# Kernel optimization log

Measured on AMD Instinct MI355X. Metric: run time of the kernel, lower is better.

Reference implementation:

```python
import jax, jax.numpy as jnp
import numpy as np
from jax import lax

ITERATIONS = 10
B, I, D, J, E = 512, 7, 512, 64, 128


def setup_inputs() -> dict:
    key = jax.random.key(0)
    k1, k2, k3 = jax.random.split(key, 3)
    f_bid = jax.random.normal(k1, (B, I, D), dtype=jnp.float32)
    p_bi = jax.random.uniform(k2, (B, I), dtype=jnp.float32)
    weights = jax.random.normal(k3, (I, D, J, E), dtype=jnp.float32)
    return {"f_bid": f_bid, "p_bi": p_bi, "weights": weights}


def reference(f_bid, p_bi, weights):
    # Precompute the per-capsule vote tensor once: [B, I, J, E]
    f_W_bije = jnp.einsum('bid,idje->bije', f_bid, weights)
    b = f_bid.shape[0]
    j, e = weights.shape[2], weights.shape[3]
    c0 = jnp.ones((b, j, e), dtype=f_bid.dtype)

    def body(c_bj, _):
        # routing logits over output capsules j, softmax over j (dim=-1 of 'bij')
        r_bij = jax.nn.softmax(jnp.einsum('bije,bje->bij', f_W_bije, c_bj), axis=-1)
        c_next = jnp.einsum('bi,bij,bije->bje', p_bi, r_bij, f_W_bije)
        return c_next, r_bij

    c_bj, r_stack = lax.scan(body, c0, None, length=ITERATIONS)
    return c_bj, r_stack[-1]
```

## Files before the change

kernel.cpp:

```cpp
#include <hip/hip_runtime.h>
#include <hip/hip_bf16.h>

#define B_SZ 512
#define I_SZ 7
#define D_SZ 512
#define J_SZ 64
#define E_SZ 128
#define N_SZ 8192
#define ITERS 10

typedef __attribute__((ext_vector_type(8))) short bf16x8;
typedef __attribute__((ext_vector_type(4))) float f32x4;

#if defined(__has_builtin)
#if __has_builtin(__builtin_amdgcn_cvt_pk_bf16_f32)
#define HAVE_CVT_PK_BF16 1
#endif
#endif

__device__ inline void split2(float x0, float x1, unsigned& hp, unsigned& lp) {
#ifdef HAVE_CVT_PK_BF16
    auto h = __builtin_amdgcn_cvt_pk_bf16_f32(x0, x1);
    hp = __builtin_bit_cast(unsigned, h);
    union { unsigned u; float f; } b0, b1;
    b0.u = hp << 16;
    b1.u = hp & 0xFFFF0000u;
    auto l = __builtin_amdgcn_cvt_pk_bf16_f32(x0 - b0.f, x1 - b1.f);
    lp = __builtin_bit_cast(unsigned, l);
#else
    union { float f; unsigned u; } u0, u1;
    u0.f = x0; u1.f = x1;
    unsigned r0 = u0.u + 0x7FFF + ((u0.u >> 16) & 1);
    unsigned r1 = u1.u + 0x7FFF + ((u1.u >> 16) & 1);
    hp = __builtin_amdgcn_perm(r1, r0, 0x07060302);
    union { unsigned u; float f; } h0, h1;
    h0.u = r0 & 0xFFFF0000u;
    h1.u = r1 & 0xFFFF0000u;
    union { float f; unsigned u; } s0, s1;
    s0.f = x0 - h0.f; s1.f = x1 - h1.f;
    unsigned q0 = s0.u + 0x7FFF + ((s0.u >> 16) & 1);
    unsigned q1 = s1.u + 0x7FFF + ((s1.u >> 16) & 1);
    lp = __builtin_amdgcn_perm(q1, q0, 0x07060302);
#endif
}

__global__ __launch_bounds__(256, 2) void vote_gemm_mfma(
    const float* __restrict__ f,
    const float* __restrict__ W,
    float* __restrict__ fW)
{
    const int i  = blockIdx.z;
    const int m0 = blockIdx.y * 128;
    const int n0 = blockIdx.x * 128;
    const int th = threadIdx.x;
    const int lane = th & 63;
    const int wave = th >> 6;
    const int wr   = wave >> 1;
    const int wc   = wave & 1;
    const int quad = lane >> 4;
    const int lm   = lane & 15;

    __shared__ short Ah_s[2][128 * 32];
    __shared__ short Al_s[2][128 * 32];
    __shared__ short Bh_s[2][128 * 32];
    __shared__ short Bl_s[2][128 * 32];

    const int sm = th >> 1;
    const int kh = th & 1;
    const int swz = (sm >> 1) & 3;
    const int wo0 = sm * 32 + (((kh << 1) | 0) ^ swz) * 8;
    const int wo1 = sm * 32 + (((kh << 1) | 1) ^ swz) * 8;

    const float* aPtr = f + (size_t)(m0 + sm) * (I_SZ * D_SZ) + (size_t)i * D_SZ + kh * 16;
    const float* bPtr = W + (size_t)i * D_SZ * N_SZ + (size_t)(kh * 16) * N_SZ + n0 + sm;

    const int fpos8 = (quad ^ ((lm >> 1) & 3)) * 8;

    f32x4 acc[4][4];
#pragma unroll
    for (int a = 0; a < 4; ++a)
#pragma unroll
        for (int c = 0; c < 4; ++c)
            acc[a][c] = (f32x4){0.f, 0.f, 0.f, 0.f};

    float av[16], bv[16];
    auto stage_load = [&](int kt) {
        const float* pa = aPtr + kt * 32;
        float4 t0 = *(const float4*)(pa);
        float4 t1 = *(const float4*)(pa + 4);
        float4 t2 = *(const float4*)(pa + 8);
        float4 t3 = *(const float4*)(pa + 12);
        av[0]=t0.x;  av[1]=t0.y;  av[2]=t0.z;  av[3]=t0.w;
        av[4]=t1.x;  av[5]=t1.y;  av[6]=t1.z;  av[7]=t1.w;
        av[8]=t2.x;  av[9]=t2.y;  av[10]=t2.z; av[11]=t2.w;
        av[12]=t3.x; av[13]=t3.y; av[14]=t3.z; av[15]=t3.w;
        const float* pb = bPtr + (size_t)kt * 32 * N_SZ;
#pragma unroll
        for (int r = 0; r < 16; ++r) bv[r] = pb[(size_t)r * N_SZ];
    };
    auto stage_write = [&](int slot) {
        short* qAh = &Ah_s[slot][0]; short* qAl = &Al_s[slot][0];
        short* qBh = &Bh_s[slot][0]; short* qBl = &Bl_s[slot][0];
        uint4 h, l;
        split2(av[0],  av[1],  h.x, l.x); split2(av[2],  av[3],  h.y, l.y);
        split2(av[4],  av[5],  h.z, l.z); split2(av[6],  av[7],  h.w, l.w);
        *(uint4*)&qAh[wo0] = h; *(uint4*)&qAl[wo0] = l;
        split2(av[8],  av[9],  h.x, l.x); split2(av[10], av[11], h.y, l.y);
        split2(av[12], av[13], h.z, l.z); split2(av[14], av[15], h.w, l.w);
        *(uint4*)&qAh[wo1] = h; *(uint4*)&qAl[wo1] = l;
        split2(bv[0],  bv[1],  h.x, l.x); split2(bv[2],  bv[3],  h.y, l.y);
        split2(bv[4],  bv[5],  h.z, l.z); split2(bv[6],  bv[7],  h.w, l.w);
        *(uint4*)&qBh[wo0] = h; *(uint4*)&qBl[wo0] = l;
        split2(bv[8],  bv[9],  h.x, l.x); split2(bv[10], bv[11], h.y, l.y);
        split2(bv[12], bv[13], h.z, l.z); split2(bv[14], bv[15], h.w, l.w);
        *(uint4*)&qBh[wo1] = h; *(uint4*)&qBl[wo1] = l;
    };

    stage_load(0);
    stage_write(0);
    __syncthreads();

    for (int t = 0; t < 16; ++t) {
        const int s = t & 1;
        const short* pAh = &Ah_s[s][0]; const short* pAl = &Al_s[s][0];
        const short* pBh = &Bh_s[s][0]; const short* pBl = &Bl_s[s][0];

        if (t < 15) stage_load(t + 1);
        __builtin_amdgcn_sched_barrier(0);

        bf16x8 Bf_h[4], Bf_l[4];
#pragma unroll
        for (int ns = 0; ns < 4; ++ns) {
            const int o = (wc * 64 + ns * 16 + lm) * 32 + fpos8;
            Bf_h[ns] = *(const bf16x8*)&pBh[o];
            Bf_l[ns] = *(const bf16x8*)&pBl[o];
        }
#pragma unroll
        for (int ms = 0; ms < 3; ++ms) {
            const int o = (wr * 64 + ms * 16 + lm) * 32 + fpos8;
            const bf16x8 Af_h = *(const bf16x8*)&pAh[o];
            const bf16x8 Af_l = *(const bf16x8*)&pAl[o];
            __builtin_amdgcn_s_setprio(1);
#pragma unroll
            for (int ns = 0; ns < 4; ++ns) {
                acc[ms][ns] = __builtin_amdgcn_mfma_f32_16x16x32_bf16(Af_h, Bf_h[ns], acc[ms][ns], 0, 0, 0);
                acc[ms][ns] = __builtin_amdgcn_mfma_f32_16x16x32_bf16(Af_h, Bf_l[ns], acc[ms][ns], 0, 0, 0);
                acc[ms][ns] = __builtin_amdgcn_mfma_f32_16x16x32_bf16(Af_l, Bf_h[ns], acc[ms][ns], 0, 0, 0);
            }
            __builtin_amdgcn_s_setprio(0);
        }
        __builtin_amdgcn_sched_barrier(0);

        if (t < 15) stage_write(s ^ 1);
        __builtin_amdgcn_sched_barrier(0);

        {
            const int o = (wr * 64 + 3 * 16 + lm) * 32 + fpos8;
            const bf16x8 Af_h = *(const bf16x8*)&pAh[o];
            const bf16x8 Af_l = *(const bf16x8*)&pAl[o];
            __builtin_amdgcn_s_setprio(1);
#pragma unroll
            for (int ns = 0; ns < 4; ++ns) {
                acc[3][ns] = __builtin_amdgcn_mfma_f32_16x16x32_bf16(Af_h, Bf_h[ns], acc[3][ns], 0, 0, 0);
                acc[3][ns] = __builtin_amdgcn_mfma_f32_16x16x32_bf16(Af_h, Bf_l[ns], acc[3][ns], 0, 0, 0);
                acc[3][ns] = __builtin_amdgcn_mfma_f32_16x16x32_bf16(Af_l, Bf_h[ns], acc[3][ns], 0, 0, 0);
            }
            __builtin_amdgcn_s_setprio(0);
        }
        __builtin_amdgcn_sched_barrier(0);

        __syncthreads();
    }

#pragma unroll
    for (int ms = 0; ms < 4; ++ms) {
        const int rowb = m0 + wr * 64 + ms * 16 + quad * 4;
#pragma unroll
        for (int ns = 0; ns < 4; ++ns) {
            const int col = n0 + wc * 64 + ns * 16 + lm;
#pragma unroll
            for (int r = 0; r < 4; ++r)
                fW[((size_t)(rowb + r) * I_SZ + i) * N_SZ + col] = acc[ms][ns][r];
        }
    }
}

__global__ __launch_bounds__(1024) void routing_kernel(
    const float* __restrict__ fW,
    const float* __restrict__ p,
    float* __restrict__ c_out,
    float* __restrict__ r_out)
{
    const int b   = blockIdx.x;
    const int tid = threadIdx.x;
    const int j   = tid >> 4;
    const int sub = tid & 15;

    __shared__ float G_sh[64][49];
    __shared__ float s_sh[64][9];
    __shared__ float w_sh[2][64][9];
    __shared__ float p_sh[8];

    if (tid < I_SZ) p_sh[tid] = p[(size_t)b * I_SZ + tid];

    float4 fw[I_SZ][2];
    const float* base = fW + (size_t)b * I_SZ * N_SZ + j * E_SZ + sub * 8;
#pragma unroll
    for (int i = 0; i < I_SZ; ++i) {
        fw[i][0] = *(const float4*)(base + (size_t)i * N_SZ);
        fw[i][1] = *(const float4*)(base + (size_t)i * N_SZ + 4);
    }

#pragma unroll
    for (int i = 0; i < I_SZ; ++i) {
        float s = fw[i][0].x + fw[i][0].y + fw[i][0].z + fw[i][0].w
                + fw[i][1].x + fw[i][1].y + fw[i][1].z + fw[i][1].w;
        s += __shfl_xor(s, 1); s += __shfl_xor(s, 2);
        s += __shfl_xor(s, 4); s += __shfl_xor(s, 8);
        if (sub == 0) s_sh[j][i] = s;
#pragma unroll
        for (int i2 = i; i2 < I_SZ; ++i2) {
            float g = fw[i][0].x * fw[i2][0].x + fw[i][0].y * fw[i2][0].y
                    + fw[i][0].z * fw[i2][0].z + fw[i][0].w * fw[i2][0].w
                    + fw[i][1].x * fw[i2][1].x + fw[i][1].y * fw[i2][1].y
                    + fw[i][1].z * fw[i2][1].z + fw[i][1].w * fw[i2][1].w;
            g += __shfl_xor(g, 1); g += __shfl_xor(g, 2);
            g += __shfl_xor(g, 4); g += __shfl_xor(g, 8);
            if (sub == 0) { G_sh[j][i * 7 + i2] = g; G_sh[j][i2 * 7 + i] = g; }
        }
    }
    __syncthreads();

    for (int t = 0; t < ITERS; ++t) {
        if (tid < I_SZ * 64) {
            const int ii = tid >> 6;
            const int jj = tid & 63;
            float l;
            if (t == 0) {
                l = s_sh[jj][ii];
            } else {
                const int rb = t & 1;
                l = 0.f;
#pragma unroll
                for (int i2 = 0; i2 < I_SZ; ++i2)
                    l = fmaf(w_sh[rb][jj][i2], G_sh[jj][ii * 7 + i2], l);
            }
            float mx = l;
#pragma unroll
            for (int off = 32; off > 0; off >>= 1)
                mx = fmaxf(mx, __shfl_xor(mx, off));
            float ex = __expf(l - mx);
            float sm = ex;
#pragma unroll
            for (int off = 32; off > 0; off >>= 1)
                sm += __shfl_xor(sm, off);
            float r = ex / sm;
            if (t == ITERS - 1)
                r_out[(size_t)b * (I_SZ * J_SZ) + ii * 64 + jj] = r;
            w_sh[(t + 1) & 1][jj][ii] = p_sh[ii] * r;
        }
        __syncthreads();
    }

    float4 a0 = make_float4(0.f, 0.f, 0.f, 0.f);
    float4 a1 = make_float4(0.f, 0.f, 0.f, 0.f);
#pragma unroll
    for (int i = 0; i < I_SZ; ++i) {
        float wv = w_sh[ITERS & 1][j][i];
        a0.x = fmaf(wv, fw[i][0].x, a0.x); a0.y = fmaf(wv, fw[i][0].y, a0.y);
        a0.z = fmaf(wv, fw[i][0].z, a0.z); a0.w = fmaf(wv, fw[i][0].w, a0.w);
        a1.x = fmaf(wv, fw[i][1].x, a1.x); a1.y = fmaf(wv, fw[i][1].y, a1.y);
        a1.z = fmaf(wv, fw[i][1].z, a1.z); a1.w = fmaf(wv, fw[i][1].w, a1.w);
    }
    float* dst = c_out + (size_t)b * N_SZ + j * E_SZ + sub * 8;
    *(float4*)(dst)     = a0;
    *(float4*)(dst + 4) = a1;
}

extern "C" void kernel_launch(void* const* d_in, const int* in_sizes, int n_in,
                              void* d_out, int out_size, void* d_ws, size_t ws_size,
                              hipStream_t stream) {
    const float* f = (const float*)d_in[0];
    const float* p = (const float*)d_in[1];
    const float* W = (const float*)d_in[2];
    float* out = (float*)d_out;
    float* fW  = (float*)d_ws;

    vote_gemm_mfma<<<dim3(N_SZ / 128, B_SZ / 128, I_SZ), 256, 0, stream>>>(f, W, fW);
    routing_kernel<<<B_SZ, 1024, 0, stream>>>(fW, p, out, out + (size_t)B_SZ * N_SZ);
}
```

Before: 327.7 us.

## Single-buffer LDS in vote GEMM and raise occupancy to four blocks per CU

Replaces the double-buffered LDS staging, where the store for the next tile was interleaved between MFMA groups, with a single LDS buffer written between two barriers each iteration. This halves LDS use per block and raises the launch-bounds occupancy hint from 2 to 4 blocks per CU, so overlap is meant to come from more resident waves rather than an in-block software pipeline. The cost is an extra barrier per k-step, a tighter register budget that could cause spills, and the removal of the explicit sched_barrier and interleaving control.

```diff
diff --git a/kernel.cpp b/kernel.cpp
--- a/kernel.cpp
+++ b/kernel.cpp
@@ -44,7 +44,7 @@
 #endif
 }
 
-__global__ __launch_bounds__(256, 2) void vote_gemm_mfma(
+__global__ __launch_bounds__(256, 4) void vote_gemm_mfma(
     const float* __restrict__ f,
     const float* __restrict__ W,
     float* __restrict__ fW)
@@ -60,10 +60,10 @@
     const int quad = lane >> 4;
     const int lm   = lane & 15;
 
-    __shared__ short Ah_s[2][128 * 32];
-    __shared__ short Al_s[2][128 * 32];
-    __shared__ short Bh_s[2][128 * 32];
-    __shared__ short Bl_s[2][128 * 32];
+    __shared__ short Ah_s[128 * 32];
+    __shared__ short Al_s[128 * 32];
+    __shared__ short Bh_s[128 * 32];
+    __shared__ short Bl_s[128 * 32];
 
     const int sm = th >> 1;
     const int kh = th & 1;
@@ -98,48 +98,41 @@
 #pragma unroll
         for (int r = 0; r < 16; ++r) bv[r] = pb[(size_t)r * N_SZ];
     };
-    auto stage_write = [&](int slot) {
-        short* qAh = &Ah_s[slot][0]; short* qAl = &Al_s[slot][0];
-        short* qBh = &Bh_s[slot][0]; short* qBl = &Bl_s[slot][0];
-        uint4 h, l;
-        split2(av[0],  av[1],  h.x, l.x); split2(av[2],  av[3],  h.y, l.y);
-        split2(av[4],  av[5],  h.z, l.z); split2(av[6],  av[7],  h.w, l.w);
-        *(uint4*)&qAh[wo0] = h; *(uint4*)&qAl[wo0] = l;
-        split2(av[8],  av[9],  h.x, l.x); split2(av[10], av[11], h.y, l.y);
-        split2(av[12], av[13], h.z, l.z); split2(av[14], av[15], h.w, l.w);
-        *(uint4*)&qAh[wo1] = h; *(uint4*)&qAl[wo1] = l;
-        split2(bv[0],  bv[1],  h.x, l.x); split2(bv[2],  bv[3],  h.y, l.y);
-        split2(bv[4],  bv[5],  h.z, l.z); split2(bv[6],  bv[7],  h.w, l.w);
-        *(uint4*)&qBh[wo0] = h; *(uint4*)&qBl[wo0] = l;
-        split2(bv[8],  bv[9],  h.x, l.x); split2(bv[10], bv[11], h.y, l.y);
-        split2(bv[12], bv[13], h.z, l.z); split2(bv[14], bv[15], h.w, l.w);
-        *(uint4*)&qBh[wo1] = h; *(uint4*)&qBl[wo1] = l;
-    };
 
     stage_load(0);
-    stage_write(0);
-    __syncthreads();
 
     for (int t = 0; t < 16; ++t) {
-        const int s = t & 1;
-        const short* pAh = &Ah_s[s][0]; const short* pAl = &Al_s[s][0];
-        const short* pBh = &Bh_s[s][0]; const short* pBl = &Bl_s[s][0];
+        uint4 ah0, al0, ah1, al1, bh0, bl0, bh1, bl1;
+        split2(av[0],  av[1],  ah0.x, al0.x); split2(av[2],  av[3],  ah0.y, al0.y);
+        split2(av[4],  av[5],  ah0.z, al0.z); split2(av[6],  av[7],  ah0.w, al0.w);
+        split2(av[8],  av[9],  ah1.x, al1.x); split2(av[10], av[11], ah1.y, al1.y);
+        split2(av[12], av[13], ah1.z, al1.z); split2(av[14], av[15], ah1.w, al1.w);
+        split2(bv[0],  bv[1],  bh0.x, bl0.x); split2(bv[2],  bv[3],  bh0.y, bl0.y);
+        split2(bv[4],  bv[5],  bh0.z, bl0.z); split2(bv[6],  bv[7],  bh0.w, bl0.w);
+        split2(bv[8],  bv[9],  bh1.x, bl1.x); split2(bv[10], bv[11], bh1.y, bl1.y);
+        split2(bv[12], bv[13], bh1.z, bl1.z); split2(bv[14], bv[15], bh1.w, bl1.w);
+
+        __syncthreads();
+        *(uint4*)&Ah_s[wo0] = ah0; *(uint4*)&Ah_s[wo1] = ah1;
+        *(uint4*)&Al_s[wo0] = al0; *(uint4*)&Al_s[wo1] = al1;
+        *(uint4*)&Bh_s[wo0] = bh0; *(uint4*)&Bh_s[wo1] = bh1;
+        *(uint4*)&Bl_s[wo0] = bl0; *(uint4*)&Bl_s[wo1] = bl1;
+        __syncthreads();
 
         if (t < 15) stage_load(t + 1);
-        __builtin_amdgcn_sched_barrier(0);
 
         bf16x8 Bf_h[4], Bf_l[4];
 #pragma unroll
         for (int ns = 0; ns < 4; ++ns) {
             const int o = (wc * 64 + ns * 16 + lm) * 32 + fpos8;
-            Bf_h[ns] = *(const bf16x8*)&pBh[o];
-            Bf_l[ns] = *(const bf16x8*)&pBl[o];
-        }
-#pragma unroll
-        for (int ms = 0; ms < 3; ++ms) {
+            Bf_h[ns] = *(const bf16x8*)&Bh_s[o];
+            Bf_l[ns] = *(const bf16x8*)&Bl_s[o];
+        }
+#pragma unroll
+        for (int ms = 0; ms < 4; ++ms) {
             const int o = (wr * 64 + ms * 16 + lm) * 32 + fpos8;
-            const bf16x8 Af_h = *(const bf16x8*)&pAh[o];
-            const bf16x8 Af_l = *(const bf16x8*)&pAl[o];
+            const bf16x8 Af_h = *(const bf16x8*)&Ah_s[o];
+            const bf16x8 Af_l = *(const bf16x8*)&Al_s[o];
             __builtin_amdgcn_s_setprio(1);
 #pragma unroll
             for (int ns = 0; ns < 4; ++ns) {
@@ -149,27 +142,6 @@
             }
             __builtin_amdgcn_s_setprio(0);
         }
-        __builtin_amdgcn_sched_barrier(0);
-
-        if (t < 15) stage_write(s ^ 1);
-        __builtin_amdgcn_sched_barrier(0);
-
-        {
-            const int o = (wr * 64 + 3 * 16 + lm) * 32 + fpos8;
-            const bf16x8 Af_h = *(const bf16x8*)&pAh[o];
-            const bf16x8 Af_l = *(const bf16x8*)&pAl[o];
-            __builtin_amdgcn_s_setprio(1);
-#pragma unroll
-            for (int ns = 0; ns < 4; ++ns) {
-                acc[3][ns] = __builtin_amdgcn_mfma_f32_16x16x32_bf16(Af_h, Bf_h[ns], acc[3][ns], 0, 0, 0);
-                acc[3][ns] = __builtin_amdgcn_mfma_f32_16x16x32_bf16(Af_h, Bf_l[ns], acc[3][ns], 0, 0, 0);
-                acc[3][ns] = __builtin_amdgcn_mfma_f32_16x16x32_bf16(Af_l, Bf_h[ns], acc[3][ns], 0, 0, 0);
-            }
-            __builtin_amdgcn_s_setprio(0);
-        }
-        __builtin_amdgcn_sched_barrier(0);
-
-        __syncthreads();
     }
 
 #pragma unroll
```

Result: slower. 554.9 us (+69.3%).
